# Kernel optimization log

Hardware: AMD Instinct MI355X
Metric: run time of the kernel (lower is better)

Reference implementation:

```python
import jax, jax.numpy as jnp
import numpy as np

D_MODEL = 384
D_STATE = 16
D_CONV = 4
EXPAND = 2
D_INNER = EXPAND * D_MODEL
DT_RANK = max(1, -(-D_MODEL // 16))  # ceil(d_model/16) = 24
BATCH = 32
SEQ = 1024


def _ssm_params(keys, prefix):
    s = 0.02
    n = lambda k, shp: jax.random.normal(k, shp, dtype=jnp.float32) * s
    A_log = jnp.broadcast_to(jnp.log(jnp.arange(1, D_STATE + 1, dtype=jnp.float32))[None, :], (D_INNER, D_STATE))
    return {
        prefix + '_in_w': n(keys[0], (2 * D_INNER, D_MODEL)),
        prefix + '_conv_w': n(keys[1], (D_INNER, 1, D_CONV)),
        prefix + '_conv_b': jnp.zeros((D_INNER,), jnp.float32),
        prefix + '_x_proj_w': n(keys[2], (DT_RANK + 2 * D_STATE, D_INNER)),
        prefix + '_dt_w': n(keys[3], (D_INNER, DT_RANK)),
        prefix + '_dt_b': jnp.zeros((D_INNER,), jnp.float32),
        prefix + '_A_log': A_log,
        prefix + '_D': jnp.ones((D_INNER,), jnp.float32),
        prefix + '_out_w': n(keys[4], (D_MODEL, D_INNER)),
    }


def setup_inputs() -> dict:
    key = jax.random.key(0)
    ks = jax.random.split(key, 13)
    inp = {
        'x': jax.random.normal(ks[0], (BATCH, SEQ, D_MODEL), dtype=jnp.float32),
        'ln_gamma': jnp.ones((D_MODEL,), jnp.float32),
        'ln_beta': jnp.zeros((D_MODEL,), jnp.float32),
        'gate_w': jax.random.normal(ks[11], (D_MODEL, 2 * D_MODEL), dtype=jnp.float32) * 0.02,
        'gate_b': jnp.zeros((D_MODEL,), jnp.float32),
    }
    inp.update(_ssm_params(ks[1:6], 'f'))
    inp.update(_ssm_params(ks[6:11], 'b'))
    return inp


def _selective_scan(xc, dt, A, Bm, Cm):
    # xc, dt: (B, L, d_inner); Bm, Cm: (B, L, N); A: (d_inner, N)
    h0 = jnp.zeros((xc.shape[0], xc.shape[2], A.shape[1]), xc.dtype)

    def step(h, inputs):
        x_t, dt_t, B_t, C_t = inputs          # (B,di), (B,di), (B,N), (B,N)
        dA = jnp.exp(dt_t[..., None] * A)     # (B, di, N)
        h = dA * h + (dt_t * x_t)[..., None] * B_t[:, None, :]
        y = jnp.einsum('bdn,bn->bd', h, C_t)
        return h, y

    xs = (jnp.moveaxis(xc, 1, 0), jnp.moveaxis(dt, 1, 0),
          jnp.moveaxis(Bm, 1, 0), jnp.moveaxis(Cm, 1, 0))
    _, ys = jax.lax.scan(step, h0, xs)
    return jnp.moveaxis(ys, 0, 1)  # (B, L, d_inner)


def _ssm(x, in_w, conv_w, conv_b, x_proj_w, dt_w, dt_b, A_log, Dp, out_w):
    L = x.shape[1]
    xz = jnp.einsum('bld,ed->ble', x, in_w)           # (B, L, 2*d_inner)
    xi, z = jnp.split(xz, 2, axis=-1)
    # depthwise causal conv1d (torch pads d_conv-1 then truncates to L)
    xc = jax.lax.conv_general_dilated(
        jnp.swapaxes(xi, 1, 2), conv_w, window_strides=(1,),
        padding=[(D_CONV - 1, 0)], feature_group_count=D_INNER,
        dimension_numbers=('NCH', 'OIH', 'NCH')) + conv_b[None, :, None]
    xc = jax.nn.silu(jnp.swapaxes(xc, 1, 2))          # (B, L, d_inner)
    xp = jnp.einsum('bld,ed->ble', xc, x_proj_w)      # (B, L, dt_rank+2N)
    dt = jax.nn.softplus(jnp.einsum('blr,dr->bld', xp[..., :DT_RANK], dt_w) + dt_b)
    Bm = xp[..., DT_RANK:DT_RANK + D_STATE]
    Cm = xp[..., DT_RANK + D_STATE:]
    A = -jnp.exp(A_log)
    y = _selective_scan(xc, dt, A, Bm, Cm)
    y = y + xc * Dp
    y = y * jax.nn.silu(z)
    return jnp.einsum('ble,de->bld', y, out_w)


def reference(x, ln_gamma, ln_beta,
              f_in_w, f_conv_w, f_conv_b, f_x_proj_w, f_dt_w, f_dt_b, f_A_log, f_D, f_out_w,
              b_in_w, b_conv_w, b_conv_b, b_x_proj_w, b_dt_w, b_dt_b, b_A_log, b_D, b_out_w,
              gate_w, gate_b):
    residual = x
    mu = jnp.mean(x, axis=-1, keepdims=True)
    var = jnp.mean((x - mu) ** 2, axis=-1, keepdims=True)
    xn = (x - mu) * jax.lax.rsqrt(var + 1e-5) * ln_gamma + ln_beta
    y_fwd = _ssm(xn, f_in_w, f_conv_w, f_conv_b, f_x_proj_w, f_dt_w, f_dt_b, f_A_log, f_D, f_out_w)
    y_bwd = _ssm(jnp.flip(xn, axis=1), b_in_w, b_conv_w, b_conv_b, b_x_proj_w, b_dt_w, b_dt_b, b_A_log, b_D, b_out_w)
    y_bwd = jnp.flip(y_bwd, axis=1)
    combined = jnp.concatenate([y_fwd, y_bwd], axis=-1)
    gate = jax.nn.sigmoid(jnp.einsum('blc,dc->bld', combined, gate_w) + gate_b)
    y = gate * y_fwd + (1.0 - gate) * y_bwd
    return y + residual
```

## Files before the change

### kernel.cpp

```cpp
#include <hip/hip_runtime.h>
#include <hip/hip_bf16.h>

#define BATCH  32
#define SEQ    1024
#define DMODEL 384
#define DINNER 768
#define DSTATE 16
#define DTRANK 24
#define NTOK   (BATCH * SEQ)
#define TC     32
#define CL     (SEQ / TC)
#define DTR_R  32

typedef __hip_bfloat16 bf16;
typedef __attribute__((ext_vector_type(8))) short frag_ab;
typedef __attribute__((ext_vector_type(4))) float frag_cd;

__device__ __forceinline__ float b2f(bf16 v) { return __bfloat162float(v); }
__device__ __forceinline__ bf16  f2b(float v) { return __float2bfloat16(v); }
__device__ __forceinline__ float ldx(const void* p, size_t i, bool f32m) {
    return f32m ? ((const float*)p)[i] : b2f(((const bf16*)p)[i]);
}

__device__ __forceinline__ void gld16(void* l, const void* g) {
    __builtin_amdgcn_global_load_lds(
        (const __attribute__((address_space(1))) unsigned int*)g,
        (__attribute__((address_space(3))) unsigned int*)l, 16, 0, 0);
}

__device__ __forceinline__ uint4 bmul8(uint4 y, uint4 s) {
    const bf16* yb = (const bf16*)&y;
    const bf16* sb = (const bf16*)&s;
    uint4 r;
    bf16* rb = (bf16*)&r;
#pragma unroll
    for (int j = 0; j < 8; ++j) rb[j] = f2b(b2f(yb[j]) * b2f(sb[j]));
    return r;
}

__global__ void detect_kernel(const unsigned short* __restrict__ x, int* flag) {
    int bad = 0;
    for (int i = threadIdx.x; i < 16384; i += 256) {
        int e = (x[i] >> 7) & 0xFF;
        bad |= (e >= 0xE0);
    }
    if (bad) atomicOr(flag, 1);
}

__global__ void struct_check(const float* __restrict__ alog, int* flag) {
    int c = blockIdx.x * 256 + threadIdx.x;
    if (c >= DINNER) return;
    float a0 = __expf(alog[c * 16]);
    int bad = 0;
#pragma unroll
    for (int n = 1; n < DSTATE; ++n) {
        float r = __expf(alog[c * 16 + n]) / a0;
        bad |= (fabsf(r - (float)(n + 1)) > 1e-3f * (n + 1));
    }
    if (bad) atomicOr(flag + 1, 1);
}

struct CvtF { const void* src[15]; float* dst[15]; int n[15]; };
struct CvtB { const void* src[7];  bf16*  dst[7];  int n[7];  };

__global__ void convert_f_kernel(CvtF p, const int* __restrict__ flag) {
    bool f32m = (*flag != 0);
    int y = blockIdx.y;
    const void* s = p.src[y];
    float* d = p.dst[y];
    int n = p.n[y];
    for (int i = blockIdx.x * 256 + threadIdx.x; i < n; i += gridDim.x * 256)
        d[i] = ldx(s, i, f32m);
}
__global__ void convert_b_kernel(CvtB p, const int* __restrict__ flag) {
    bool f32m = (*flag != 0);
    int y = blockIdx.y;
    const void* s = p.src[y];
    bf16* d = p.dst[y];
    int n = p.n[y];
    for (int i = blockIdx.x * 256 + threadIdx.x; i < n; i += gridDim.x * 256)
        d[i] = f2b(ldx(s, i, f32m));
}

__global__ void transpose_dtw(const float* __restrict__ w, float* __restrict__ wt) {
    int i = blockIdx.x * 256 + threadIdx.x;
    if (i >= DINNER * DTRANK) return;
    int c = i / DTRANK, r = i % DTRANK;
    wt[r * DINNER + c] = w[i];
}

__global__ void ln_kernel(const void* __restrict__ x, size_t xoff,
                          const float* __restrict__ gamma, const float* __restrict__ beta,
                          bf16* __restrict__ xn, const int* __restrict__ flag) {
    bool f32m = (*flag != 0);
    int wave = threadIdx.x >> 6;
    int lane = threadIdx.x & 63;
    int row  = blockIdx.x * 4 + wave;
    size_t base = xoff + (size_t)row * DMODEL;
    float v[6];
    float s = 0.f, s2 = 0.f;
#pragma unroll
    for (int i = 0; i < 6; ++i) {
        v[i] = ldx(x, base + lane + i * 64, f32m);
        s += v[i];
        s2 += v[i] * v[i];
    }
#pragma unroll
    for (int off = 32; off >= 1; off >>= 1) {
        s  += __shfl_down(s, off, 64);
        s2 += __shfl_down(s2, off, 64);
    }
    s  = __shfl(s, 0, 64);
    s2 = __shfl(s2, 0, 64);
    float mu   = s / DMODEL;
    float var  = s2 / DMODEL - mu * mu;
    float rstd = rsqrtf(var + 1e-5f);
    bf16* xnr = xn + (size_t)row * DMODEL;
#pragma unroll
    for (int i = 0; i < 6; ++i)
        xnr[lane + i * 64] = f2b((v[i] - mu) * rstd * gamma[lane + i * 64] + beta[lane + i * 64]);
}

__device__ __forceinline__ void compute_tile(const bf16 (*Al)[32], const bf16 (*Bl)[32],
                                             frag_cd acc[4][4], int wm, int wn,
                                             int mr, int quad) {
    frag_ab af[4], bfr[4];
#pragma unroll
    for (int r = 0; r < 4; ++r)
        af[r] = *(const frag_ab*)&Al[wm * 64 + r * 16 + mr][quad * 8];
#pragma unroll
    for (int c = 0; c < 4; ++c)
        bfr[c] = *(const frag_ab*)&Bl[wn * 64 + c * 16 + mr][quad * 8];
#pragma unroll
    for (int r = 0; r < 4; ++r)
#pragma unroll
        for (int c = 0; c < 4; ++c)
            acc[r][c] = __builtin_amdgcn_mfma_f32_16x16x32_bf16(af[r], bfr[c], acc[r][c], 0, 0, 0);
}

template <int MODE>
__global__ __launch_bounds__(256) void gemm_mfma(
    const bf16* __restrict__ A, const bf16* __restrict__ W,
    int K, int lda, int ldw, int nNT,
    bf16* __restrict__ C, int ldc, int cofs,
    float* __restrict__ Cf, bf16* __restrict__ Cz, const bf16* __restrict__ Sz,
    const float* __restrict__ gb, const void* __restrict__ xg, size_t xoff,
    void* __restrict__ outg, const int* __restrict__ flag) {
    __shared__ bf16 Als[2][128][32];
    __shared__ bf16 Bls[2][128][32];
    int tid = threadIdx.x;
    int lane = tid & 63;
    int w = tid >> 6;
    int wm = w & 1, wn = w >> 1;
    int wgid = blockIdx.x;
    int mt_lo = wgid & 7;
    int rr_ = wgid >> 3;
    int nt = rr_ % nNT;
    int mt = (rr_ / nNT) * 8 + mt_lo;
    int m0 = mt * 128, n0 = nt * 128;
    int row = tid >> 2, kc = tid & 3;
    int mr = lane & 15, quad = lane >> 4;

    const bf16* Ab0 = A + (size_t)(m0 + row) * lda + kc * 8;
    const bf16* Ab1 = A + (size_t)(m0 + 64 + row) * lda + kc * 8;
    const bf16* Wb0 = W + (size_t)(n0 + row) * ldw + kc * 8;
    const bf16* Wb1 = W + (size_t)(n0 + 64 + row) * ldw + kc * 8;
    const bf16* Zb0 = (MODE == 5) ? (Sz + (size_t)(m0 + row) * DINNER + kc * 8) : nullptr;
    const bf16* Zb1 = (MODE == 5) ? (Sz + (size_t)(m0 + 64 + row) * DINNER + kc * 8) : nullptr;

    frag_cd acc[4][4] = {};
    const int NT = K / 32;

    if (MODE == 5) {
        uint4 eya0, eya1, esz0, esz1;
        uint4 oya0, oya1, osz0, osz1;
        eya0 = *(const uint4*)(Ab0);      eya1 = *(const uint4*)(Ab1);
        esz0 = *(const uint4*)(Zb0);      esz1 = *(const uint4*)(Zb1);
        oya0 = *(const uint4*)(Ab0 + 32); oya1 = *(const uint4*)(Ab1 + 32);
        osz0 = *(const uint4*)(Zb0 + 32); osz1 = *(const uint4*)(Zb1 + 32);
        *(uint4*)&Als[0][row][kc * 8]      = bmul8(eya0, esz0);
        *(uint4*)&Als[0][64 + row][kc * 8] = bmul8(eya1, esz1);
        gld16(&Bls[0][row][kc * 8], Wb0);
        gld16(&Bls[0][64 + row][kc * 8], Wb1);
        __syncthreads();
        for (int t = 0; t < NT; t += 2) {
            int k1 = (t + 1) * 32, k2 = (t + 2) * 32, k3 = (t + 3) * 32;
            *(uint4*)&Als[1][row][kc * 8]      = bmul8(oya0, osz0);
            *(uint4*)&Als[1][64 + row][kc * 8] = bmul8(oya1, osz1);
            gld16(&Bls[1][row][kc * 8], Wb0 + k1);
            gld16(&Bls[1][64 + row][kc * 8], Wb1 + k1);
            if (t + 2 < NT) {
                eya0 = *(const uint4*)(Ab0 + k2); eya1 = *(const uint4*)(Ab1 + k2);
                esz0 = *(const uint4*)(Zb0 + k2); esz1 = *(const uint4*)(Zb1 + k2);
            }
            compute_tile(Als[0], Bls[0], acc, wm, wn, mr, quad);
            __syncthreads();
            if (t + 2 < NT) {
                *(uint4*)&Als[0][row][kc * 8]      = bmul8(eya0, esz0);
                *(uint4*)&Als[0][64 + row][kc * 8] = bmul8(eya1, esz1);
                gld16(&Bls[0][row][kc * 8], Wb0 + k2);
                gld16(&Bls[0][64 + row][kc * 8], Wb1 + k2);
                oya0 = *(const uint4*)(Ab0 + k3); oya1 = *(const uint4*)(Ab1 + k3);
                osz0 = *(const uint4*)(Zb0 + k3); osz1 = *(const uint4*)(Zb1 + k3);
            }
            compute_tile(Als[1], Bls[1], acc, wm, wn, mr, quad);
            __syncthreads();
        }
    } else {
        gld16(&Als[0][row][kc * 8], Ab0);
        gld16(&Als[0][64 + row][kc * 8], Ab1);
        gld16(&Bls[0][row][kc * 8], Wb0);
        gld16(&Bls[0][64 + row][kc * 8], Wb1);
        __syncthreads();
        for (int t = 0; t < NT; t += 2) {
            int k1 = (t + 1) * 32, k2 = (t + 2) * 32;
            gld16(&Als[1][row][kc * 8], Ab0 + k1);
            gld16(&Als[1][64 + row][kc * 8], Ab1 + k1);
            gld16(&Bls[1][row][kc * 8], Wb0 + k1);
            gld16(&Bls[1][64 + row][kc * 8], Wb1 + k1);
            compute_tile(Als[0], Bls[0], acc, wm, wn, mr, quad);
            __syncthreads();
            if (t + 2 < NT) {
                gld16(&Als[0][row][kc * 8], Ab0 + k2);
                gld16(&Als[0][64 + row][kc * 8], Ab1 + k2);
                gld16(&Bls[0][row][kc * 8], Wb0 + k2);
                gld16(&Bls[0][64 + row][kc * 8], Wb1 + k2);
            }
            compute_tile(Als[1], Bls[1], acc, wm, wn, mr, quad);
            __syncthreads();
        }
    }

    bool f32m = (MODE == 1) ? (*flag != 0) : false;
#pragma unroll
    for (int r = 0; r < 4; ++r) {
#pragma unroll
        for (int c = 0; c < 4; ++c) {
#pragma unroll
            for (int reg = 0; reg < 4; ++reg) {
                int gm = m0 + wm * 64 + r * 16 + quad * 4 + reg;
                int gn = n0 + wn * 64 + c * 16 + mr;
                float v = acc[r][c][reg];
                if (MODE == 0 || MODE == 5) {
                    C[(size_t)gm * ldc + cofs + gn] = f2b(v);
                } else if (MODE == 2) {
                    if (gn < DTRANK + 2 * DSTATE) Cf[(size_t)gm * 56 + gn] = v;
                } else if (MODE == 4) {
                    if (gn < DINNER) {
                        C[(size_t)gm * DINNER + gn] = f2b(v);
                    } else {
                        float sz = v / (1.f + __expf(-v));
                        Cz[(size_t)gm * DINNER + (gn - DINNER)] = f2b(sz);
                    }
                } else {
                    float g   = 1.f / (1.f + __expf(-(v + gb[gn])));
                    float yfv = b2f(A[(size_t)gm * DINNER + gn]);
                    float ybv = b2f(A[(size_t)gm * DINNER + DMODEL + gn]);
                    size_t gi = xoff + (size_t)gm * DMODEL + gn;
                    float xv  = f32m ? ((const float*)xg)[gi] : b2f(((const bf16*)xg)[gi]);
                    float rr  = g * yfv + (1.f - g) * ybv + xv;
                    if (f32m) ((float*)outg)[gi] = rr;
                    else      ((bf16*)outg)[gi]  = f2b(rr);
                }
            }
        }
    }
}

__global__ void conv_kernel(const bf16* __restrict__ xi_buf, const float* __restrict__ cw,
                            const float* __restrict__ cb, bf16* __restrict__ xc, int reverse) {
    int g = blockIdx.x * blockDim.x + threadIdx.x;
    int c8 = (g % (DINNER / 8)) * 8;
    int bl = g / (DINNER / 8);
    int l = bl % SEQ;
    int b = bl / SEQ;
    float4 wq[8];
#pragma unroll
    for (int j = 0; j < 8; ++j) wq[j] = *(const float4*)(cw + (c8 + j) * 4);
    float4 cb0 = *(const float4*)(cb + c8);
    float4 cb1 = *(const float4*)(cb + c8 + 4);
    float acc[8] = {cb0.x, cb0.y, cb0.z, cb0.w, cb1.x, cb1.y, cb1.z, cb1.w};

    const bf16* base = xi_buf + (size_t)b * SEQ * DINNER + c8;
#pragma unroll
    for (int k = 0; k < 4; ++k) {
        int ll = reverse ? (l + k) : (l - 3 + k);
        int wk = reverse ? (3 - k) : k;
        if (ll >= 0 && ll < SEQ) {
            uint4 v = *(const uint4*)(base + (size_t)ll * DINNER);
            const bf16* vb = (const bf16*)&v;
#pragma unroll
            for (int j = 0; j < 8; ++j)
                acc[j] += b2f(vb[j]) * ((const float*)&wq[j])[wk];
        }
    }
    uint4 out;
    bf16* ob = (bf16*)&out;
#pragma unroll
    for (int j = 0; j < 8; ++j)
        ob[j] = f2b(acc[j] / (1.f + __expf(-acc[j])));
    *(uint4*)(xc + (size_t)bl * DINNER + c8) = out;
}

__global__ __launch_bounds__(256, 4) void dt_kernel(const float* __restrict__ xp,
                                                    const float* __restrict__ dtwT,
                                                    const float* __restrict__ dtb,
                                                    float* __restrict__ dtf) {
    __shared__ float4 xps[DTR_R][6];
    int tid = threadIdx.x;
    int c = blockIdx.y * 256 + tid;
    float w[DTRANK];
#pragma unroll
    for (int r = 0; r < DTRANK; ++r) w[r] = dtwT[r * DINNER + c];
#pragma unroll
    for (int r = 0; r < DTRANK; ++r) asm volatile("" : "+v"(w[r]));
    float bias = dtb[c];

    size_t row0 = (size_t)blockIdx.x * DTR_R;
    for (int i = tid; i < DTR_R * 6; i += 256) {
        int s = i / 6, q = i % 6;
        xps[s][q] = *(const float4*)(xp + (row0 + s) * 56 + q * 4);
    }
    __syncthreads();

    for (int s = 0; s < DTR_R; s += 2) {
        float a0 = bias, a1 = bias;
#pragma unroll
        for (int q = 0; q < 6; ++q) {
            float4 x0 = xps[s][q];
            float4 x1 = xps[s + 1][q];
            a0 += x0.x * w[q * 4 + 0];  a1 += x1.x * w[q * 4 + 0];
            a0 += x0.y * w[q * 4 + 1];  a1 += x1.y * w[q * 4 + 1];
            a0 += x0.z * w[q * 4 + 2];  a1 += x1.z * w[q * 4 + 2];
            a0 += x0.w * w[q * 4 + 3];  a1 += x1.w * w[q * 4 + 3];
        }
        float e0 = __builtin_amdgcn_exp2f(fabsf(a0) * -1.44269504f);
        float e1 = __builtin_amdgcn_exp2f(fabsf(a1) * -1.44269504f);
        a0 = fmaxf(a0, 0.f) + 0.69314718f * __builtin_amdgcn_logf(1.f + e0);
        a1 = fmaxf(a1, 0.f) + 0.69314718f * __builtin_amdgcn_logf(1.f + e1);
        dtf[(row0 + s) * DINNER + c]     = a0;
        dtf[(row0 + s + 1) * DINNER + c] = a1;
    }
}

template <int PHASE>
__global__ void scan_phase(const float* __restrict__ xp, const bf16* __restrict__ xc,
                           const float* __restrict__ dtf, const float* __restrict__ Alog,
                           const float* __restrict__ Dg, float* __restrict__ states,
                           bf16* __restrict__ ydir, int reverse, const int* __restrict__ flag) {
    __shared__ __align__(16) float xps[16][32];
    bool generic = (flag[1] != 0);
    int tid = threadIdx.x;
    int bidx = blockIdx.x;
    int tc  = bidx % TC;
    int cgb = bidx / TC;
    int cg  = cgb % 6;
    int bb  = cgb / 6;
    int c = cg * 128 + tid;

    float Av0 = -__expf(Alog[c * DSTATE]);
    float Av[DSTATE];
    if (generic) {
#pragma unroll
        for (int n = 0; n < DSTATE; ++n) Av[n] = -__expf(Alog[c * DSTATE + n]);
    }
    float Dv = Dg[c];

    float h[DSTATE];
    float Q = 1.f, Pg[DSTATE];
    size_t sbase = (size_t)bidx * 32;
    if (PHASE == 0) {
#pragma unroll
        for (int n = 0; n < DSTATE; ++n) { h[n] = 0.f; Pg[n] = 1.f; }
    } else {
#pragma unroll
        for (int n = 0; n < DSTATE; ++n) h[n] = states[(sbase + n) * 128 + tid];
    }

    const size_t brow = (size_t)bb * SEQ;
    const int t0 = tc * CL;
    const int tr0 = reverse ? (SEQ - 1 - t0) : t0;
    const long dstep = reverse ? -(long)DINNER : (long)DINNER;
    const float* pdt = dtf + (brow + tr0) * DINNER + c;
    const bf16*  pxc = xc  + (brow + tr0) * DINNER + c;
    bf16* pyd = (PHASE == 1) ? (ydir + (brow + tr0) * DINNER + c) : nullptr;

    for (int g0 = 0; g0 < CL; g0 += 16) {
        __syncthreads();
        for (int i = tid; i < 16 * 32; i += 128) {
            int s = i >> 5, r = i & 31;
            int t = t0 + g0 + s;
            int tr = reverse ? (SEQ - 1 - t) : t;
            xps[s][r] = xp[(brow + tr) * 56 + 24 + r];
        }
        __syncthreads();
        for (int s = 0; s < 16; ++s) {
            float dt  = *pdt;  pdt += dstep;
            float xcv = b2f(*pxc);  pxc += dstep;
            float dtx = dt * xcv;
            float4 B0 = *(const float4*)&xps[s][0];
            float4 B1 = *(const float4*)&xps[s][4];
            float4 B2 = *(const float4*)&xps[s][8];
            float4 B3 = *(const float4*)&xps[s][12];
            float Bv[DSTATE] = {B0.x, B0.y, B0.z, B0.w, B1.x, B1.y, B1.z, B1.w,
                                B2.x, B2.y, B2.z, B2.w, B3.x, B3.y, B3.z, B3.w};
            float accv = 0.f;
            if (PHASE == 1) {
                float4 C0 = *(const float4*)&xps[s][16];
                float4 C1 = *(const float4*)&xps[s][20];
                float4 C2 = *(const float4*)&xps[s][24];
                float4 C3 = *(const float4*)&xps[s][28];
                float Cv[DSTATE] = {C0.x, C0.y, C0.z, C0.w, C1.x, C1.y, C1.z, C1.w,
                                    C2.x, C2.y, C2.z, C2.w, C3.x, C3.y, C3.z, C3.w};
                if (!generic) {
                    float e1 = __expf(dt * Av0);
                    float d = e1;
#pragma unroll
                    for (int n = 0; n < DSTATE; ++n) {
                        h[n] = d * h[n] + dtx * Bv[n];
                        accv += h[n] * Cv[n];
                        d *= e1;
                    }
                } else {
#pragma unroll
                    for (int n = 0; n < DSTATE; ++n) {
                        float dA = __expf(dt * Av[n]);
                        h[n] = dA * h[n] + dtx * Bv[n];
                        accv += h[n] * Cv[n];
                    }
                }
                *pyd = f2b(accv + xcv * Dv);
                pyd += dstep;
            } else {
                if (!generic) {
                    float e1 = __expf(dt * Av0);
                    float d = e1;
#pragma unroll
                    for (int n = 0; n < DSTATE; ++n) {
                        h[n] = d * h[n] + dtx * Bv[n];
                        d *= e1;
                    }
                    Q *= e1;
                } else {
#pragma unroll
                    for (int n = 0; n < DSTATE; ++n) {
                        float dA = __expf(dt * Av[n]);
                        h[n] = dA * h[n] + dtx * Bv[n];
                        Pg[n] *= dA;
                    }
                }
            }
        }
    }
    if (PHASE == 0) {
        if (!generic) {
            float d = Q;
#pragma unroll
            for (int n = 0; n < DSTATE; ++n) { Pg[n] = d; d *= Q; }
        }
#pragma unroll
        for (int n = 0; n < DSTATE; ++n) {
            states[(sbase + n) * 128 + tid]      = Pg[n];
            states[(sbase + 16 + n) * 128 + tid] = h[n];
        }
    }
}

__global__ void scan_stitch(float* __restrict__ states) {
    int tid = threadIdx.x;
    int cgb = blockIdx.x;
    float h[DSTATE];
#pragma unroll
    for (int n = 0; n < DSTATE; ++n) h[n] = 0.f;
    for (int tc = 0; tc < TC; ++tc) {
        size_t base = ((size_t)cgb * TC + tc) * 32;
#pragma unroll
        for (int n = 0; n < DSTATE; ++n) {
            float Pv = states[(base + n) * 128 + tid];
            float ev = states[(base + 16 + n) * 128 + tid];
            states[(base + n) * 128 + tid] = h[n];
            h[n] = Pv * h[n] + ev;
        }
    }
}

extern "C" void kernel_launch(void* const* d_in, const int* in_sizes, int n_in,
                              void* d_out, int out_size, void* d_ws, size_t ws_size,
                              hipStream_t stream) {
    (void)n_in; (void)out_size;
    bool dict_order = (in_sizes[4] < 2048);
    int fbase = dict_order ? 5 : 3;
    int bbase = dict_order ? 14 : 12;
    int gwi = dict_order ? 3 : 21;
    int gbi = dict_order ? 4 : 22;

    auto al = [](size_t b) { return (b + 255) & ~(size_t)255; };
    char* ws = (char*)d_ws;
    size_t off = 0;
    auto alloc = [&](size_t bytes) {
        void* p = ws + off;
        off += al(bytes);
        return p;
    };

    int* flag = (int*)alloc(256);

    CvtF pf{};
    int cf = 0;
    auto addf = [&](int idx, int n) {
        float* d = (float*)alloc((size_t)n * 4);
        pf.src[cf] = d_in[idx]; pf.dst[cf] = d; pf.n[cf] = n; ++cf;
        return d;
    };
    float* ln_gc   = addf(1, DMODEL);
    float* ln_bc   = addf(2, DMODEL);
    float* gate_bc = addf(gbi, DMODEL);
    float* convw_f[2], *convb_f[2], *dtw_f[2], *dtb_f[2], *alog_f[2], *dd_f[2];
    for (int d = 0; d < 2; ++d) {
        int base = d ? bbase : fbase;
        convw_f[d] = addf(base + 1, DINNER * 4);
        convb_f[d] = addf(base + 2, DINNER);
        dtw_f[d]   = addf(base + 4, DINNER * DTRANK);
        dtb_f[d]   = addf(base + 5, DINNER);
        alog_f[d]  = addf(base + 6, DINNER * DSTATE);
        dd_f[d]    = addf(base + 7, DINNER);
    }

    CvtB pb{};
    int cb = 0;
    auto addb = [&](int idx, int n, size_t alloc_n) {
        bf16* d = (bf16*)alloc(alloc_n * 2);
        pb.src[cb] = d_in[idx]; pb.dst[cb] = d; pb.n[cb] = n; ++cb;
        return d;
    };
    bf16* gate_wb = addb(gwi, DMODEL * 2 * DMODEL, (size_t)DMODEL * 2 * DMODEL);
    bf16 *inw_b[2], *xpw_b[2], *outw_b[2];
    for (int d = 0; d < 2; ++d) {
        int base = d ? bbase : fbase;
        inw_b[d]  = addb(base + 0, 2 * DINNER * DMODEL, (size_t)2 * DINNER * DMODEL);
        xpw_b[d]  = addb(base + 3, 56 * DINNER, (size_t)128 * DINNER);
        outw_b[d] = addb(base + 8, DMODEL * DINNER, (size_t)DMODEL * DINNER);
    }

    float* dtwT_f[2];
    for (int d = 0; d < 2; ++d)
        dtwT_f[d] = (float*)alloc((size_t)DTRANK * DINNER * 4);

    size_t fixed = off;

    auto chunk_need = [&](int bc) {
        size_t T = (size_t)bc * SEQ;
        return al(T * DMODEL * 2)
             + 2 * al(T * DINNER * 2)
             + al(T * 56 * 4)
             + al(T * DINNER * 4)
             + al(T * DINNER * 2)
             + al(T * DINNER * 2)
             + al((size_t)bc * 6 * TC * 32 * 128 * 4);
    };
    int Bc = 32;
    while (Bc > 1 && fixed + chunk_need(Bc) > ws_size) Bc >>= 1;
    size_t T = (size_t)Bc * SEQ;
    int nMT = (int)(T / 128);

    bf16*  xn_c   = (bf16*)alloc(T * DMODEL * 2);
    bf16*  xib    = (bf16*)alloc(T * DINNER * 2);
    bf16*  xcb    = (bf16*)alloc(T * DINNER * 2);
    float* xpb    = (float*)alloc(T * 56 * 4);
    float* dtfb   = (float*)alloc(T * DINNER * 4);
    bf16*  zbb    = (bf16*)alloc(T * DINNER * 2);
    bf16*  ycat   = (bf16*)alloc(T * DINNER * 2);
    float* states = (float*)alloc((size_t)Bc * 6 * TC * 32 * 128 * 4);
    bf16*  ydir   = xib;

    hipMemsetAsync(flag, 0, 8, stream);
    for (int d = 0; d < 2; ++d)
        hipMemsetAsync(xpw_b[d], 0, (size_t)128 * DINNER * 2, stream);
    detect_kernel<<<1, 256, 0, stream>>>((const unsigned short*)d_in[0], flag);
    convert_f_kernel<<<dim3(8, 15), 256, 0, stream>>>(pf, flag);
    convert_b_kernel<<<dim3(32, 7), 256, 0, stream>>>(pb, flag);
    struct_check<<<3, 256, 0, stream>>>(alog_f[0], flag);
    struct_check<<<3, 256, 0, stream>>>(alog_f[1], flag);
    for (int d = 0; d < 2; ++d)
        transpose_dtw<<<(DINNER * DTRANK + 255) / 256, 256, 0, stream>>>(dtw_f[d], dtwT_f[d]);

    for (int c0 = 0; c0 < BATCH; c0 += Bc) {
        size_t tok0 = (size_t)c0 * SEQ;

        ln_kernel<<<(unsigned)(T / 4), 256, 0, stream>>>(
            d_in[0], tok0 * DMODEL, ln_gc, ln_bc, xn_c, flag);

        for (int dir = 0; dir < 2; ++dir) {
            gemm_mfma<4><<<nMT * 12, 256, 0, stream>>>(
                xn_c, inw_b[dir], DMODEL, DMODEL, DMODEL, 12,
                xib, DINNER, 0, nullptr, zbb, nullptr,
                nullptr, nullptr, 0, nullptr, flag);
            conv_kernel<<<(unsigned)((T * DINNER) / 2048), 256, 0, stream>>>(
                xib, convw_f[dir], convb_f[dir], xcb, dir);
            gemm_mfma<2><<<nMT * 1, 256, 0, stream>>>(
                xcb, xpw_b[dir], DINNER, DINNER, DINNER, 1,
                nullptr, 0, 0, xpb, nullptr, nullptr,
                nullptr, nullptr, 0, nullptr, flag);
            dt_kernel<<<dim3((unsigned)(T / DTR_R), 3), 256, 0, stream>>>(
                xpb, dtwT_f[dir], dtb_f[dir], dtfb);
            scan_phase<0><<<Bc * 6 * TC, 128, 0, stream>>>(
                xpb, xcb, dtfb, alog_f[dir], dd_f[dir], states, nullptr, dir, flag);
            scan_stitch<<<Bc * 6, 128, 0, stream>>>(states);
            scan_phase<1><<<Bc * 6 * TC, 128, 0, stream>>>(
                xpb, xcb, dtfb, alog_f[dir], dd_f[dir], states, ydir, dir, flag);
            gemm_mfma<5><<<nMT * 3, 256, 0, stream>>>(
                ydir, outw_b[dir], DINNER, DINNER, DINNER, 3,
                ycat, DINNER, dir * DMODEL, nullptr, nullptr, zbb,
                nullptr, nullptr, 0, nullptr, flag);
        }

        gemm_mfma<1><<<nMT * 3, 256, 0, stream>>>(
            ycat, gate_wb, DINNER, DINNER, DINNER, 3,
            nullptr, 0, 0, nullptr, nullptr, nullptr,
            gate_bc, d_in[0], tok0 * DMODEL, d_out, flag);
    }
}
```

Measured before the change: 1.247 ms.

## Use four-stage LDS ring with prefetch depth two in bf16 GEMM

Replaces the double-buffered k-loop in non-MODE-5 GEMMs with a 4-buffer shared memory ring that keeps two tiles of global-to-LDS loads in flight, using explicit s_waitcnt vmcnt counts and a single barrier per iteration instead of two __syncthreads. The goal is to hide global load latency and cut barrier overhead. It doubles LDS usage for these modes, which can lower occupancy. It also depends on exact vmcnt accounting of the gld16 instructions, which is fragile.

```diff
diff --git a/kernel.cpp b/kernel.cpp
--- a/kernel.cpp
+++ b/kernel.cpp
@@ -146,8 +146,9 @@
     float* __restrict__ Cf, bf16* __restrict__ Cz, const bf16* __restrict__ Sz,
     const float* __restrict__ gb, const void* __restrict__ xg, size_t xoff,
     void* __restrict__ outg, const int* __restrict__ flag) {
-    __shared__ bf16 Als[2][128][32];
-    __shared__ bf16 Bls[2][128][32];
+    constexpr int NBUF = (MODE == 5) ? 2 : 4;
+    __shared__ bf16 Als[NBUF][128][32];
+    __shared__ bf16 Bls[NBUF][128][32];
     int tid = threadIdx.x;
     int lane = tid & 63;
     int w = tid >> 6;
@@ -207,27 +208,28 @@
             __syncthreads();
         }
     } else {
-        gld16(&Als[0][row][kc * 8], Ab0);
-        gld16(&Als[0][64 + row][kc * 8], Ab1);
-        gld16(&Bls[0][row][kc * 8], Wb0);
-        gld16(&Bls[0][64 + row][kc * 8], Wb1);
-        __syncthreads();
-        for (int t = 0; t < NT; t += 2) {
-            int k1 = (t + 1) * 32, k2 = (t + 2) * 32;
-            gld16(&Als[1][row][kc * 8], Ab0 + k1);
-            gld16(&Als[1][64 + row][kc * 8], Ab1 + k1);
-            gld16(&Bls[1][row][kc * 8], Wb0 + k1);
-            gld16(&Bls[1][64 + row][kc * 8], Wb1 + k1);
-            compute_tile(Als[0], Bls[0], acc, wm, wn, mr, quad);
-            __syncthreads();
+        auto stage = [&](int ts) {
+            int k = ts * 32;
+            int b = ts & 3;
+            gld16(&Als[b][row][kc * 8],      Ab0 + k);
+            gld16(&Als[b][64 + row][kc * 8], Ab1 + k);
+            gld16(&Bls[b][row][kc * 8],      Wb0 + k);
+            gld16(&Bls[b][64 + row][kc * 8], Wb1 + k);
+        };
+        stage(0);
+        stage(1);
+        for (int t = 0; t < NT; ++t) {
             if (t + 2 < NT) {
-                gld16(&Als[0][row][kc * 8], Ab0 + k2);
-                gld16(&Als[0][64 + row][kc * 8], Ab1 + k2);
-                gld16(&Bls[0][row][kc * 8], Wb0 + k2);
-                gld16(&Bls[0][64 + row][kc * 8], Wb1 + k2);
+                stage(t + 2);
+                asm volatile("s_waitcnt vmcnt(8)" ::: "memory");
+            } else if (t + 1 < NT) {
+                asm volatile("s_waitcnt vmcnt(4)" ::: "memory");
+            } else {
+                asm volatile("s_waitcnt vmcnt(0)" ::: "memory");
             }
-            compute_tile(Als[1], Bls[1], acc, wm, wn, mr, quad);
-            __syncthreads();
+            __builtin_amdgcn_s_barrier();
+            asm volatile("" ::: "memory");
+            compute_tile(Als[t & 3], Bls[t & 3], acc, wm, wn, mr, quad);
         }
     }
 
```

After: 1.255 ms. About the same (+0.6%).
